# Performance work log

Measured on AMD Instinct MI355X. Metric: run time of the kernel, lower is better.

The kernel has to match this reference:

```python
import jax, jax.numpy as jnp
import numpy as np

P, N, B, F, H, O, D, A = 3, 6144, 3072, 512, 8, 32, 256, 128
HI = F // H  # per-head input dim = 64


def setup_inputs() -> dict:
    key = jax.random.key(0)
    ks = jax.random.split(key, 12)
    s = 0.05
    return dict(
        features=jax.random.normal(ks[0], (P, N, F), jnp.float32),
        biases=jax.random.normal(ks[1], (P, N, N), jnp.float32),
        batch_nodes=jax.random.randint(ks[2], (P, B), 0, N),
        RL_thresholds=jax.random.uniform(ks[3], (P, 1), jnp.float32),
        Wc1=jax.random.normal(ks[4], (P, H, O, HI), jnp.float32) * s,
        bc1=jnp.zeros((P, H, O), jnp.float32),
        a1=jax.random.normal(ks[5], (P, H, O), jnp.float32) * s,
        ab1=jnp.zeros((P, H), jnp.float32),
        a2=jax.random.normal(ks[6], (P, H, O), jnp.float32) * s,
        ab2=jnp.zeros((P, H), jnp.float32),
        Wm=jax.random.normal(ks[7], (D, D), jnp.float32) * s,
        bm=jnp.zeros((D,), jnp.float32),
        w_omega=jax.random.normal(ks[8], (D, A), jnp.float32) * s,
        b_omega=jnp.zeros((A,), jnp.float32),
        u_omega=jax.random.normal(ks[9], (A,), jnp.float32) * s,
    )


def reference(features, biases, batch_nodes, RL_thresholds, Wc1, bc1, a1, ab1,
              a2, ab2, Wm, bm, w_omega, b_omega, u_omega):
    embeds = []
    for i in range(P):  # fixed small relation loop (bias_mx_len)
        idx = batch_nodes[i]
        bf = features[i][idx]                      # [B, F]
        bb = biases[i][idx][:, idx]                # [B, B] bias mask
        xh = bf.reshape(B, H, HI).transpose(1, 0, 2)   # [H, B, HI] per-head feature slices
        # Attn_Head: conv1d(k=1) == per-head linear projection
        seq = jnp.einsum('hbi,hoi->hbo', xh, Wc1[i]) + bc1[i][:, None, :]  # [H, B, O]
        f1 = jnp.einsum('hbo,ho->hb', seq, a1[i]) + ab1[i][:, None]       # [H, B]
        f2 = jnp.einsum('hbo,ho->hb', seq, a2[i]) + ab2[i][:, None]       # [H, B]
        logits = jax.nn.leaky_relu(f1[:, :, None] + f2[:, None, :], 0.01)  # [H, B, B]
        coefs = jax.nn.softmax(logits + bb[None], axis=-1)                 # [H, B, B]
        out = jax.nn.elu(jnp.einsum('hqk,hko->hqo', coefs, seq))           # [H, B, O]
        h1 = out.transpose(1, 0, 2).reshape(B, H * O)                      # concat heads -> [B, D]
        embeds.append(h1 @ Wm.T + bm)                                      # w_multi
    multi = jnp.stack(embeds, axis=1)              # [B, P, D]
    inputs = multi * RL_thresholds[None]           # RL scaling, [P,1] broadcasts
    # SimpleAttnLayer: semantic attention over relations
    v = jnp.tanh(jnp.einsum('bpd,da->bpa', inputs, w_omega) + b_omega)
    vu = jnp.einsum('bpa,a->bp', v, u_omega)
    alphas = jax.nn.softmax(vu, axis=-1)           # [B, P]
    return jnp.sum(inputs * alphas[:, :, None], axis=1)  # [B, D]
```

## Files before the change

kernel.cpp:

```cpp
#include <hip/hip_runtime.h>
#include <hip/hip_bf16.h>
#include <cstdint>
#include <cstddef>

#define PP 3
#define NN 6144
#define BB 3072
#define FF 512
#define HH 8
#define OO 32
#define DD 256
#define AA 128
#define M0 10.0f
#define KSPLIT 4
#define KRANGE (BB/KSPLIT)
#define NT (KRANGE/32)

typedef __attribute__((ext_vector_type(8))) short short8;
typedef __attribute__((ext_vector_type(4))) float f32x4;

__device__ __forceinline__ unsigned short f2bf(float x){
  union { float f; unsigned u; } v; v.f = x;
  unsigned r = v.u + 0x7fffu + ((v.u >> 16) & 1u);
  return (unsigned short)(r >> 16);
}

__device__ __forceinline__ short f2bf_n(float x){
  return __builtin_bit_cast(short, __float2bfloat16(x));
}

__device__ __forceinline__ f32x4 mfma16(short8 a, short8 b, f32x4 c){
  return __builtin_amdgcn_mfma_f32_16x16x32_bf16(a, b, c, 0, 0, 0);
}

__global__ __launch_bounds__(256) void k_seq(
    const float* __restrict__ features, const int* __restrict__ batch_nodes,
    const float* __restrict__ Wc1, const float* __restrict__ bc1,
    const float* __restrict__ a1, const float* __restrict__ ab1,
    const float* __restrict__ a2, const float* __restrict__ ab2,
    unsigned short* __restrict__ seqT, float* __restrict__ f1g, float* __restrict__ f2T)
{
  int i = blockIdx.z, h = blockIdx.y, b0 = blockIdx.x * 8;
  int t = threadIdx.x;
  __shared__ float xs[8][64];
  __shared__ float wt[64][33];
  __shared__ float a1s[32], a2s[32], bcs[32];
  __shared__ float sst[32][9];
  const float* W = Wc1 + (size_t)(i*HH + h) * OO * 64;
  for (int e = t; e < 2048; e += 256){ int o = e >> 6, c = e & 63; wt[c][o] = W[e]; }
  if (t < 32){
    a1s[t] = a1[(i*HH+h)*OO + t];
    a2s[t] = a2[(i*HH+h)*OO + t];
    bcs[t] = bc1[(i*HH+h)*OO + t];
  }
  for (int e = t; e < 512; e += 256){
    int bl = e >> 6, c = e & 63;
    int row = batch_nodes[i*BB + b0 + bl];
    xs[bl][c] = features[((size_t)i*NN + row)*FF + h*64 + c];
  }
  __syncthreads();
  int bl = t >> 5, o = t & 31;
  float acc = bcs[o];
  #pragma unroll
  for (int c = 0; c < 64; c++) acc += xs[bl][c] * wt[c][o];
  float v1 = acc * a1s[o], v2 = acc * a2s[o];
  #pragma unroll
  for (int s = 16; s >= 1; s >>= 1){ v1 += __shfl_xor(v1, s); v2 += __shfl_xor(v2, s); }
  if (o == 0){
    f1g[(i*HH+h)*BB + b0 + bl] = v1 + ab1[i*HH+h];
    f2T[((size_t)i*BB + b0 + bl)*HH + h] = v2 + ab2[i*HH+h];
  }
  sst[o][bl] = acc;
  __syncthreads();
  {
    int o2 = t >> 3, b2 = t & 7;
    seqT[((size_t)(i*HH+h)*OO + o2)*BB + b0 + b2] = f2bf(sst[o2][b2]);
  }
}

__global__ __launch_bounds__(256) void k_gather(
    const float* __restrict__ biases, const int* __restrict__ batch_nodes,
    float* __restrict__ bbg, int i_base, int nbuf)
{
  int i = i_base + blockIdx.z;
  int q0 = blockIdx.x * 2;
  int t = threadIdx.x;
  __shared__ float rowbuf[2][NN];
  int r0 = batch_nodes[i*BB + q0];
  int r1 = batch_nodes[i*BB + q0 + 1];
  const float4* s0 = (const float4*)(biases + ((size_t)i*NN + r0)*NN);
  const float4* s1 = (const float4*)(biases + ((size_t)i*NN + r1)*NN);
  #pragma unroll
  for (int e = 0; e < NN/4; e += 256){
    ((float4*)rowbuf[0])[e + t] = s0[e + t];
    ((float4*)rowbuf[1])[e + t] = s1[e + t];
  }
  const int* ci = batch_nodes + i*BB;
  float* dst0 = bbg + ((size_t)(i % nbuf)*BB + q0)*BB;
  float* dst1 = dst0 + BB;
  __syncthreads();
  #pragma unroll 4
  for (int c = 0; c < BB; c += 256){
    int k = c + t;
    int col = ci[k];
    dst0[k] = rowbuf[0][col] - M0;
    dst1[k] = rowbuf[1][col] - M0;
  }
}

__global__ __launch_bounds__(256, 4) void k_attn(
    const float* __restrict__ bbg, const unsigned short* __restrict__ seqT,
    const float* __restrict__ f1g, const float* __restrict__ f2T,
    float* __restrict__ Lp, float* __restrict__ h1p, int i_base, int nbuf)
{
  int i = i_base + blockIdx.z;
  int ks = blockIdx.y;
  int q0 = blockIdx.x * 32;
  int kbase = ks * KRANGE;
  int t = threadIdx.x;
  int w = t >> 6, lane = t & 63;
  int qf = lane & 15, kq = lane >> 4;
  __shared__ float bbt[2][32][33];
  __shared__ float f2t[2][32][9];
  f32x4 acc[2][2][2] = {};
  float Ls[2][2] = {{0.f,0.f},{0.f,0.f}};
  float f1r[2][2];
  #pragma unroll
  for (int hh = 0; hh < 2; hh++)
  #pragma unroll
  for (int qh = 0; qh < 2; qh++){
    int h = w*2 + hh;
    f1r[hh][qh] = f1g[(i*HH+h)*BB + q0 + qh*16 + qf];
  }
  const float* bbb = bbg + (size_t)(i % nbuf)*BB*BB;

  auto ld = [&](int k0, float rb[4], float &rf, short8 rs[4]){
    #pragma unroll
    for (int j = 0; j < 4; j++){ int e = j*256 + t; int r = e >> 5, c = e & 31;
      rb[j] = bbb[(size_t)(q0 + r)*BB + k0 + c]; }
    { int c = t >> 3, h = t & 7; rf = f2T[((size_t)i*BB + k0 + c)*HH + h]; }
    #pragma unroll
    for (int hh = 0; hh < 2; hh++){
      const unsigned short* sp = seqT + ((size_t)(i*HH + w*2 + hh)*OO)*BB + k0 + kq*8;
      rs[hh*2+0] = *(const short8*)(sp + (size_t)qf*BB);
      rs[hh*2+1] = *(const short8*)(sp + (size_t)(qf+16)*BB);
    }
  };
  auto st = [&](int buf, float rb[4], float rf){
    #pragma unroll
    for (int j = 0; j < 4; j++){ int e = j*256 + t; int r = e >> 5, c = e & 31; bbt[buf][r][c] = rb[j]; }
    { int c = t >> 3, h = t & 7; f2t[buf][c][h] = rf; }
  };
  auto comp = [&](int buf, short8 rs[4]){
    #pragma unroll
    for (int hh = 0; hh < 2; hh++){
      int h = w*2 + hh;
      int kk = kq*8;
      short8 af0, af1;
      #pragma unroll
      for (int j = 0; j < 8; j++){
        float f2v = f2t[buf][kk+j][h];
        float s0 = f1r[hh][0] + f2v; s0 = (s0 >= 0.f ? s0 : 0.01f*s0) + bbt[buf][qf][kk+j];
        float s1 = f1r[hh][1] + f2v; s1 = (s1 >= 0.f ? s1 : 0.01f*s1) + bbt[buf][qf+16][kk+j];
        float e0 = __expf(s0), e1 = __expf(s1);
        Ls[hh][0] += e0; Ls[hh][1] += e1;
        af0[j] = f2bf_n(e0);
        af1[j] = f2bf_n(e1);
      }
      acc[hh][0][0] = mfma16(af0, rs[hh*2+0], acc[hh][0][0]);
      acc[hh][0][1] = mfma16(af0, rs[hh*2+1], acc[hh][0][1]);
      acc[hh][1][0] = mfma16(af1, rs[hh*2+0], acc[hh][1][0]);
      acc[hh][1][1] = mfma16(af1, rs[hh*2+1], acc[hh][1][1]);
    }
  };

  float rbbA[4], rf2A; short8 rsqA[4];
  float rbbB[4], rf2B; short8 rsqB[4];
  ld(kbase, rbbA, rf2A, rsqA);
  st(0, rbbA, rf2A);
  __syncthreads();
  for (int it = 0; it < NT; it += 2){
    int k1 = kbase + (it+1)*32;
    int k2 = (it+2 < NT) ? kbase + (it+2)*32 : kbase;
    ld(k1, rbbB, rf2B, rsqB);
    comp(0, rsqA);
    st(1, rbbB, rf2B);
    __syncthreads();
    ld(k2, rbbA, rf2A, rsqA);
    comp(1, rsqB);
    st(0, rbbA, rf2A);
    __syncthreads();
  }
  #pragma unroll
  for (int hh = 0; hh < 2; hh++)
  #pragma unroll
  for (int qh = 0; qh < 2; qh++){
    float v = Ls[hh][qh];
    v += __shfl_xor(v, 16);
    v += __shfl_xor(v, 32);
    if (kq == 0)
      Lp[(((size_t)ks*PP + i)*HH + w*2 + hh)*BB + q0 + qh*16 + qf] = v;
  }
  #pragma unroll
  for (int hh = 0; hh < 2; hh++){
    int h = w*2 + hh;
    #pragma unroll
    for (int qh = 0; qh < 2; qh++)
    #pragma unroll
    for (int oh = 0; oh < 2; oh++)
    #pragma unroll
    for (int r = 0; r < 4; r++){
      int q = q0 + qh*16 + kq*4 + r;
      int o = qf + oh*16;
      h1p[(((size_t)ks*PP + i)*BB + q)*DD + h*OO + o] = acc[hh][qh][oh][r];
    }
  }
}

__global__ __launch_bounds__(256) void k_twm(const float* __restrict__ Wm, float* __restrict__ wmT){
  int e = blockIdx.x, d = threadIdx.x;
  wmT[(size_t)e*DD + d] = Wm[(size_t)d*DD + e];
}

__global__ __launch_bounds__(256) void k_final(
    const float* __restrict__ h1p, const float* __restrict__ Lp,
    const float* __restrict__ wmT, const float* __restrict__ bm,
    const float* __restrict__ RL, const float* __restrict__ w_omega, const float* __restrict__ b_omega,
    const float* __restrict__ u_omega, float* __restrict__ out)
{
  __shared__ float buf[48*256];
  __shared__ float wred[4][24];
  __shared__ float alph[3][16];
  __shared__ float linvs[48][8];
  const size_t PB = (size_t)PP*BB*DD;
  const size_t KL = (size_t)PP*HH*BB;
  int t = threadIdx.x;
  int lane = t & 63, w = t >> 6;
  int b0 = blockIdx.x * 16;
  for (int e = t; e < 48*8; e += 256){
    int pb = e >> 3, h = e & 7;
    int p = pb / 16, bl = pb & 15;
    size_t off = ((size_t)p*HH + h)*BB + b0 + bl;
    float L = Lp[off] + Lp[off+KL] + Lp[off+2*KL] + Lp[off+3*KL];
    linvs[pb][h] = 1.f / L;
  }
  __syncthreads();
  for (int e = t; e < 48*256; e += 256){
    int pb = e >> 8, d = e & 255;
    int p = pb / 16, bl = pb & 15;
    size_t off = ((size_t)p*BB + b0 + bl)*DD + d;
    float v = h1p[off] + h1p[off + PB] + h1p[off + 2*PB] + h1p[off + 3*PB];
    v *= linvs[pb][d >> 5];
    buf[e] = (v > 0.f) ? v : (__expf(v) - 1.f);
  }
  __syncthreads();
  float acc[48];
  #pragma unroll
  for (int x = 0; x < 48; x++) acc[x] = 0.f;
  for (int e = 0; e < 256; e += 4){
    float w0 = wmT[(e+0)*DD + t];
    float w1 = wmT[(e+1)*DD + t];
    float w2 = wmT[(e+2)*DD + t];
    float w3 = wmT[(e+3)*DD + t];
    #pragma unroll
    for (int pb = 0; pb < 48; pb++){
      float4 hv = *(const float4*)&buf[pb*256 + e];
      acc[pb] += hv.x*w0 + hv.y*w1 + hv.z*w2 + hv.w*w3;
    }
  }
  __syncthreads();
  {
    float bmv = bm[t];
    #pragma unroll
    for (int p = 0; p < 3; p++){
      float rl = RL[p];
      #pragma unroll
      for (int bl = 0; bl < 16; bl++)
        buf[(p*16+bl)*256 + t] = (acc[p*16+bl] + bmv) * rl;
    }
  }
  __syncthreads();
  int a = t & 127, g = t >> 7;
  float acc2[24];
  #pragma unroll
  for (int x = 0; x < 24; x++) acc2[x] = 0.f;
  for (int e = 0; e < 256; e += 4){
    float w0 = w_omega[(e+0)*AA + a];
    float w1 = w_omega[(e+1)*AA + a];
    float w2 = w_omega[(e+2)*AA + a];
    float w3 = w_omega[(e+3)*AA + a];
    #pragma unroll
    for (int p = 0; p < 3; p++){
      #pragma unroll
      for (int bl = 0; bl < 8; bl++){
        float4 iv = *(const float4*)&buf[(p*16 + g*8 + bl)*256 + e];
        acc2[p*8+bl] += iv.x*w0 + iv.y*w1 + iv.z*w2 + iv.w*w3;
      }
    }
  }
  {
    float bo = b_omega[a], uo = u_omega[a];
    #pragma unroll
    for (int x = 0; x < 24; x++){
      float v = tanhf(acc2[x] + bo) * uo;
      #pragma unroll
      for (int s = 32; s >= 1; s >>= 1) v += __shfl_xor(v, s);
      if (lane == 0) wred[w][x] = v;
    }
  }
  __syncthreads();
  if (t < 16){
    int b = t;
    int g2 = b >> 3, bl2 = b & 7;
    float vu[3];
    #pragma unroll
    for (int p = 0; p < 3; p++){
      int j = p*8 + bl2;
      vu[p] = wred[g2*2 + 0][j] + wred[g2*2 + 1][j];
    }
    float mx = fmaxf(vu[0], fmaxf(vu[1], vu[2]));
    float e0 = __expf(vu[0]-mx), e1 = __expf(vu[1]-mx), e2 = __expf(vu[2]-mx);
    float inv = 1.f / (e0+e1+e2);
    alph[0][b] = e0*inv; alph[1][b] = e1*inv; alph[2][b] = e2*inv;
  }
  __syncthreads();
  #pragma unroll
  for (int bl = 0; bl < 16; bl++){
    float o = buf[(0*16+bl)*256 + t]*alph[0][bl]
            + buf[(1*16+bl)*256 + t]*alph[1][bl]
            + buf[(2*16+bl)*256 + t]*alph[2][bl];
    out[(size_t)(b0+bl)*DD + t] = o;
  }
}

extern "C" void kernel_launch(void* const* d_in, const int* in_sizes, int n_in,
                              void* d_out, int out_size, void* d_ws, size_t ws_size,
                              hipStream_t stream)
{
  const float* features = (const float*)d_in[0];
  const float* biases   = (const float*)d_in[1];
  const int*   batch_nodes = (const int*)d_in[2];
  const float* RL   = (const float*)d_in[3];
  const float* Wc1  = (const float*)d_in[4];
  const float* bc1  = (const float*)d_in[5];
  const float* a1   = (const float*)d_in[6];
  const float* ab1  = (const float*)d_in[7];
  const float* a2   = (const float*)d_in[8];
  const float* ab2  = (const float*)d_in[9];
  const float* Wm   = (const float*)d_in[10];
  const float* bm   = (const float*)d_in[11];
  const float* w_omega = (const float*)d_in[12];
  const float* b_omega = (const float*)d_in[13];
  const float* u_omega = (const float*)d_in[14];
  float* out = (float*)d_out;

  size_t sz_bbg1 = (size_t)BB*BB*4;
  size_t sz_seqT = (size_t)PP*HH*OO*BB*2;
  size_t sz_f    = (size_t)PP*HH*BB*4;
  size_t sz_h1   = (size_t)PP*BB*DD*4;
  size_t sz_wmT  = (size_t)DD*DD*4;
  size_t sz_Lp   = (size_t)KSPLIT*PP*HH*BB*4;
  size_t fixed = sz_seqT + 2*sz_f + (size_t)KSPLIT*sz_h1 + sz_wmT + sz_Lp + 16*256;
  int nbuf = (ws_size >= fixed + 3*sz_bbg1 + 256) ? 3 : 1;

  char* p = (char*)d_ws;
  auto take = [&](size_t bytes)->char*{ char* r = p; p += (bytes + 255) & ~(size_t)255; return r; };
  float* bbg  = (float*)take(sz_bbg1 * (size_t)nbuf);
  unsigned short* seqT = (unsigned short*)take(sz_seqT);
  float* f1g  = (float*)take(sz_f);
  float* f2T  = (float*)take(sz_f);
  float* Lp   = (float*)take(sz_Lp);
  float* h1p  = (float*)take(sz_h1 * (size_t)KSPLIT);
  float* wmT  = (float*)take(sz_wmT);

  k_twm<<<dim3(DD), dim3(DD), 0, stream>>>(Wm, wmT);
  k_seq<<<dim3(BB/8, HH, PP), dim3(256), 0, stream>>>(features, batch_nodes, Wc1, bc1, a1, ab1, a2, ab2, seqT, f1g, f2T);
  int nloop = (nbuf == 3) ? 1 : 3;
  int z = (nbuf == 3) ? 3 : 1;
  for (int r = 0; r < nloop; r++){
    k_gather<<<dim3(BB/2, 1, z), dim3(256), 0, stream>>>(biases, batch_nodes, bbg, r, nbuf);
    k_attn<<<dim3(BB/32, KSPLIT, z), dim3(256), 0, stream>>>(bbg, seqT, f1g, f2T, Lp, h1p, r, nbuf);
  }
  k_final<<<dim3(BB/16), dim3(256), 0, stream>>>(h1p, Lp, wmT, bm, RL, w_omega, b_omega, u_omega, out);
}
```

Baseline: 1.093 ms.

## Load attention tiles straight to registers, drop LDS staging, use exp2 with prescaled logits

The attention kernel no longer stages the bias and f2 tiles through shared memory with barriers. Each lane now loads its own bias rows and f2 values with vector loads straight into registers and double-buffers them in a register Tile struct. f2 is stored head-major so the loads are contiguous. Logits and bias are prescaled by log2(e) upstream so the kernel can use the hardware exp2 builtin, and leaky ReLU becomes fmaxf. This removes the LDS round trips and __syncthreads, but the extra registers lower the occupancy hint from 4 to 3 blocks, and each lane's loads now cover redundant data across waves.

```diff
diff --git a/kernel.cpp b/kernel.cpp
--- a/kernel.cpp
+++ b/kernel.cpp
@@ -1,5 +1,4 @@
 #include <hip/hip_runtime.h>
-#include <hip/hip_bf16.h>
 #include <cstdint>
 #include <cstddef>
 
@@ -12,6 +11,7 @@
 #define DD 256
 #define AA 128
 #define M0 10.0f
+#define LOG2E 1.44269504088896340736f
 #define KSPLIT 4
 #define KRANGE (BB/KSPLIT)
 #define NT (KRANGE/32)
@@ -25,8 +25,12 @@
   return (unsigned short)(r >> 16);
 }
 
-__device__ __forceinline__ short f2bf_n(float x){
-  return __builtin_bit_cast(short, __float2bfloat16(x));
+__device__ __forceinline__ float fexp2(float x){
+#if __has_builtin(__builtin_amdgcn_exp2f)
+  return __builtin_amdgcn_exp2f(x);
+#else
+  return exp2f(x);
+#endif
 }
 
 __device__ __forceinline__ f32x4 mfma16(short8 a, short8 b, f32x4 c){
@@ -38,7 +42,7 @@
     const float* __restrict__ Wc1, const float* __restrict__ bc1,
     const float* __restrict__ a1, const float* __restrict__ ab1,
     const float* __restrict__ a2, const float* __restrict__ ab2,
-    unsigned short* __restrict__ seqT, float* __restrict__ f1g, float* __restrict__ f2T)
+    unsigned short* __restrict__ seqT, float* __restrict__ f1g, float* __restrict__ f2g)
 {
   int i = blockIdx.z, h = blockIdx.y, b0 = blockIdx.x * 8;
   int t = threadIdx.x;
@@ -67,8 +71,8 @@
   #pragma unroll
   for (int s = 16; s >= 1; s >>= 1){ v1 += __shfl_xor(v1, s); v2 += __shfl_xor(v2, s); }
   if (o == 0){
-    f1g[(i*HH+h)*BB + b0 + bl] = v1 + ab1[i*HH+h];
-    f2T[((size_t)i*BB + b0 + bl)*HH + h] = v2 + ab2[i*HH+h];
+    f1g[(i*HH+h)*BB + b0 + bl] = (v1 + ab1[i*HH+h]) * LOG2E;
+    f2g[(i*HH+h)*BB + b0 + bl] = (v2 + ab2[i*HH+h]) * LOG2E;
   }
   sst[o][bl] = acc;
   __syncthreads();
@@ -103,14 +107,14 @@
   for (int c = 0; c < BB; c += 256){
     int k = c + t;
     int col = ci[k];
-    dst0[k] = rowbuf[0][col] - M0;
-    dst1[k] = rowbuf[1][col] - M0;
-  }
-}
-
-__global__ __launch_bounds__(256, 4) void k_attn(
+    dst0[k] = (rowbuf[0][col] - M0) * LOG2E;
+    dst1[k] = (rowbuf[1][col] - M0) * LOG2E;
+  }
+}
+
+__global__ __launch_bounds__(256, 3) void k_attn(
     const float* __restrict__ bbg, const unsigned short* __restrict__ seqT,
-    const float* __restrict__ f1g, const float* __restrict__ f2T,
+    const float* __restrict__ f1g, const float* __restrict__ f2g,
     float* __restrict__ Lp, float* __restrict__ h1p, int i_base, int nbuf)
 {
   int i = i_base + blockIdx.z;
@@ -120,8 +124,6 @@
   int t = threadIdx.x;
   int w = t >> 6, lane = t & 63;
   int qf = lane & 15, kq = lane >> 4;
-  __shared__ float bbt[2][32][33];
-  __shared__ float f2t[2][32][9];
   f32x4 acc[2][2][2] = {};
   float Ls[2][2] = {{0.f,0.f},{0.f,0.f}};
   float f1r[2][2];
@@ -133,64 +135,66 @@
     f1r[hh][qh] = f1g[(i*HH+h)*BB + q0 + qh*16 + qf];
   }
   const float* bbb = bbg + (size_t)(i % nbuf)*BB*BB;
-
-  auto ld = [&](int k0, float rb[4], float &rf, short8 rs[4]){
-    #pragma unroll
-    for (int j = 0; j < 4; j++){ int e = j*256 + t; int r = e >> 5, c = e & 31;
-      rb[j] = bbb[(size_t)(q0 + r)*BB + k0 + c]; }
-    { int c = t >> 3, h = t & 7; rf = f2T[((size_t)i*BB + k0 + c)*HH + h]; }
+  const float* bbp0 = bbb + (size_t)(q0 + qf)*BB + kbase + kq*8;
+  const float* bbp1 = bbp0 + (size_t)16*BB;
+  const float* f2p0 = f2g + ((size_t)(i*HH + w*2 + 0))*BB + kbase + kq*8;
+  const float* f2p1 = f2p0 + BB;
+  const unsigned short* sq00 = seqT + ((size_t)(i*HH + w*2 + 0)*OO + qf)*BB + kbase + kq*8;
+  const unsigned short* sq01 = sq00 + (size_t)16*BB;
+  const unsigned short* sq10 = sq00 + (size_t)OO*BB;
+  const unsigned short* sq11 = sq10 + (size_t)16*BB;
+
+  struct Tile {
+    f32x4 bb[2][2];
+    f32x4 f2[2][2];
+    short8 sq[2][2];
+  };
+  auto loadt = [&](Tile &T, int d){
+    #pragma unroll
+    for (int c = 0; c < 2; c++){
+      T.bb[0][c] = *(const f32x4*)(bbp0 + d + c*4);
+      T.bb[1][c] = *(const f32x4*)(bbp1 + d + c*4);
+      T.f2[0][c] = *(const f32x4*)(f2p0 + d + c*4);
+      T.f2[1][c] = *(const f32x4*)(f2p1 + d + c*4);
+    }
+    T.sq[0][0] = *(const short8*)(sq00 + d);
+    T.sq[0][1] = *(const short8*)(sq01 + d);
+    T.sq[1][0] = *(const short8*)(sq10 + d);
+    T.sq[1][1] = *(const short8*)(sq11 + d);
+  };
+  auto compt = [&](const Tile &T){
     #pragma unroll
     for (int hh = 0; hh < 2; hh++){
-      const unsigned short* sp = seqT + ((size_t)(i*HH + w*2 + hh)*OO)*BB + k0 + kq*8;
-      rs[hh*2+0] = *(const short8*)(sp + (size_t)qf*BB);
-      rs[hh*2+1] = *(const short8*)(sp + (size_t)(qf+16)*BB);
-    }
-  };
-  auto st = [&](int buf, float rb[4], float rf){
-    #pragma unroll
-    for (int j = 0; j < 4; j++){ int e = j*256 + t; int r = e >> 5, c = e & 31; bbt[buf][r][c] = rb[j]; }
-    { int c = t >> 3, h = t & 7; f2t[buf][c][h] = rf; }
-  };
-  auto comp = [&](int buf, short8 rs[4]){
-    #pragma unroll
-    for (int hh = 0; hh < 2; hh++){
-      int h = w*2 + hh;
-      int kk = kq*8;
       short8 af0, af1;
       #pragma unroll
       for (int j = 0; j < 8; j++){
-        float f2v = f2t[buf][kk+j][h];
-        float s0 = f1r[hh][0] + f2v; s0 = (s0 >= 0.f ? s0 : 0.01f*s0) + bbt[buf][qf][kk+j];
-        float s1 = f1r[hh][1] + f2v; s1 = (s1 >= 0.f ? s1 : 0.01f*s1) + bbt[buf][qf+16][kk+j];
-        float e0 = __expf(s0), e1 = __expf(s1);
+        float f2v = T.f2[hh][j>>2][j&3];
+        float s0 = f1r[hh][0] + f2v;
+        s0 = fmaxf(s0, 0.01f*s0) + T.bb[0][j>>2][j&3];
+        float s1 = f1r[hh][1] + f2v;
+        s1 = fmaxf(s1, 0.01f*s1) + T.bb[1][j>>2][j&3];
+        float e0 = fexp2(s0);
+        float e1 = fexp2(s1);
         Ls[hh][0] += e0; Ls[hh][1] += e1;
-        af0[j] = f2bf_n(e0);
-        af1[j] = f2bf_n(e1);
+        af0[j] = (short)f2bf(e0);
+        af1[j] = (short)f2bf(e1);
       }
-      acc[hh][0][0] = mfma16(af0, rs[hh*2+0], acc[hh][0][0]);
-      acc[hh][0][1] = mfma16(af0, rs[hh*2+1], acc[hh][0][1]);
-      acc[hh][1][0] = mfma16(af1, rs[hh*2+0], acc[hh][1][0]);
-      acc[hh][1][1] = mfma16(af1, rs[hh*2+1], acc[hh][1][1]);
+      acc[hh][0][0] = mfma16(af0, T.sq[hh][0], acc[hh][0][0]);
+      acc[hh][0][1] = mfma16(af0, T.sq[hh][1], acc[hh][0][1]);
+      acc[hh][1][0] = mfma16(af1, T.sq[hh][0], acc[hh][1][0]);
+      acc[hh][1][1] = mfma16(af1, T.sq[hh][1], acc[hh][1][1]);
     }
   };
 
-  float rbbA[4], rf2A; short8 rsqA[4];
-  float rbbB[4], rf2B; short8 rsqB[4];
-  ld(kbase, rbbA, rf2A, rsqA);
-  st(0, rbbA, rf2A);
-  __syncthreads();
+  Tile ta, tb;
+  loadt(ta, 0);
   for (int it = 0; it < NT; it += 2){
-    int k1 = kbase + (it+1)*32;
-    int k2 = (it+2 < NT) ? kbase + (it+2)*32 : kbase;
-    ld(k1, rbbB, rf2B, rsqB);
-    comp(0, rsqA);
-    st(1, rbbB, rf2B);
-    __syncthreads();
-    ld(k2, rbbA, rf2A, rsqA);
-    comp(1, rsqB);
-    st(0, rbbA, rf2A);
-    __syncthreads();
-  }
+    loadt(tb, (it+1)*32);
+    compt(ta);
+    if (it + 2 < NT) loadt(ta, (it+2)*32);
+    compt(tb);
+  }
+
   #pragma unroll
   for (int hh = 0; hh < 2; hh++)
   #pragma unroll
@@ -368,18 +372,18 @@
   float* bbg  = (float*)take(sz_bbg1 * (size_t)nbuf);
   unsigned short* seqT = (unsigned short*)take(sz_seqT);
   float* f1g  = (float*)take(sz_f);
-  float* f2T  = (float*)take(sz_f);
+  float* f2g  = (float*)take(sz_f);
   float* Lp   = (float*)take(sz_Lp);
   float* h1p  = (float*)take(sz_h1 * (size_t)KSPLIT);
   float* wmT  = (float*)take(sz_wmT);
 
   k_twm<<<dim3(DD), dim3(DD), 0, stream>>>(Wm, wmT);
-  k_seq<<<dim3(BB/8, HH, PP), dim3(256), 0, stream>>>(features, batch_nodes, Wc1, bc1, a1, ab1, a2, ab2, seqT, f1g, f2T);
+  k_seq<<<dim3(BB/8, HH, PP), dim3(256), 0, stream>>>(features, batch_nodes, Wc1, bc1, a1, ab1, a2, ab2, seqT, f1g, f2g);
   int nloop = (nbuf == 3) ? 1 : 3;
   int z = (nbuf == 3) ? 3 : 1;
   for (int r = 0; r < nloop; r++){
     k_gather<<<dim3(BB/2, 1, z), dim3(256), 0, stream>>>(biases, batch_nodes, bbg, r, nbuf);
-    k_attn<<<dim3(BB/32, KSPLIT, z), dim3(256), 0, stream>>>(bbg, seqT, f1g, f2T, Lp, h1p, r, nbuf);
+    k_attn<<<dim3(BB/32, KSPLIT, z), dim3(256), 0, stream>>>(bbg, seqT, f1g, f2g, Lp, h1p, r, nbuf);
   }
   k_final<<<dim3(BB/16), dim3(256), 0, stream>>>(h1p, Lp, wmT, bm, RL, w_omega, b_omega, u_omega, out);
 }
```

New measurement: 961.8 us. -12.0%, faster.
